# Kernel tuning notes

Measured on AMD Instinct MI355X. Metric: run time of the kernel, lower is better.

Reference implementation:

```python
import jax, jax.numpy as jnp
import numpy as np

B, C, H, W = 4, 256, 64, 64
PD = 32  # projection_dim = in_channels // projection_ratio


def setup_inputs() -> dict:
    key = jax.random.key(0)
    ks = jax.random.split(key, 7)
    x = jax.random.normal(ks[0], (B, C, H, W), dtype=jnp.float32)
    Wq = jax.random.normal(ks[1], (PD, C), dtype=jnp.float32) * (1.0 / np.sqrt(C))
    bq = jax.random.normal(ks[2], (PD,), dtype=jnp.float32) * 0.01
    Wk = jax.random.normal(ks[3], (PD, C), dtype=jnp.float32) * (1.0 / np.sqrt(C))
    bk = jax.random.normal(ks[4], (PD,), dtype=jnp.float32) * 0.01
    Wv = jax.random.normal(ks[5], (C, C), dtype=jnp.float32) * (1.0 / np.sqrt(C))
    bv = jax.random.normal(ks[6], (C,), dtype=jnp.float32) * 0.01
    gamma = jnp.float32(1.0)
    return {"x": x, "Wq": Wq, "bq": bq, "Wk": Wk, "bk": bk, "Wv": Wv, "bv": bv, "gamma": gamma}


def reference(x, Wq, bq, Wk, bk, Wv, bv, gamma):
    b, c, h, w = x.shape
    xf = x.reshape(b, c, h * w)                      # [B, C, N]
    q = jnp.einsum('dc,bcn->bnd', Wq, xf) + bq       # [B, N, PD]
    k = jnp.einsum('dc,bcn->bdn', Wk, xf) + bk[:, None]   # [B, PD, N]
    v = jnp.einsum('ec,bcn->ben', Wv, xf) + bv[:, None]   # [B, C, N]
    scores = jnp.einsum('bnd,bdm->bnm', q, k)        # [B, N, N] (no scaling, per original)
    attn = jax.nn.softmax(scores, axis=-1)           # softmax over keys
    out = jnp.einsum('bcn,bmn->bcm', v, attn)        # v @ attn^T -> [B, C, N]
    out = out.reshape(b, c, h, w)
    return gamma * out + x
```

## Files before the change

### kernel.cpp

```cpp
#include <hip/hip_runtime.h>
#include <stdint.h>

typedef _Float16 half_t;
typedef __attribute__((ext_vector_type(8))) _Float16 f16x8;
typedef __attribute__((ext_vector_type(4))) _Float16 f16x4;
typedef __attribute__((ext_vector_type(2))) __fp16 fp16x2;
typedef __attribute__((ext_vector_type(4))) float f32x4;
typedef __attribute__((ext_vector_type(16))) float f32x16;
typedef __attribute__((ext_vector_type(4))) uint32_t u32x4;
typedef __attribute__((ext_vector_type(2))) int i32x2;

#define DEVI __device__ __forceinline__

static constexpr int Bn = 4, Cc = 256, Nn = 4096, PD = 32;
static constexpr float L2E = 1.44269504089f;

__device__ half_t g_Q[(size_t)Bn * Nn * PD];
__device__ half_t g_K[(size_t)Bn * Nn * PD];
__device__ half_t g_V[(size_t)Bn * Cc * Nn];

DEVI f16x8 cvt8(float4 a, float4 b) {
    f16x8 r;
    r[0] = (_Float16)a.x; r[1] = (_Float16)a.y; r[2] = (_Float16)a.z; r[3] = (_Float16)a.w;
    r[4] = (_Float16)b.x; r[5] = (_Float16)b.y; r[6] = (_Float16)b.z; r[7] = (_Float16)b.w;
    return r;
}

DEVI uint32_t pkrtz(float a, float b) {
    fp16x2 h = __builtin_amdgcn_cvt_pkrtz(a, b);
    return __builtin_bit_cast(uint32_t, h);
}

DEVI float asf(int u) { return __builtin_bit_cast(float, u); }
DEVI int   asi(float f) { return __builtin_bit_cast(int, f); }

DEVI i32x2 pl32swap(int a, int b) {
    return __builtin_amdgcn_permlane32_swap(a, b, false, false);
}

DEVI void gll16(const void* g, void* l) {
    auto gp = (const __attribute__((address_space(1))) uint32_t*)(uintptr_t)g;
    auto lp = (__attribute__((address_space(3))) uint32_t*)(uintptr_t)l;
    __builtin_amdgcn_global_load_lds(gp, lp, 16, 0, 0);
}

__global__ __launch_bounds__(256, 1) void proj_kernel(
    const float* __restrict__ x,
    const float* __restrict__ Wq, const float* __restrict__ bq,
    const float* __restrict__ Wk, const float* __restrict__ bk,
    const float* __restrict__ Wv, const float* __restrict__ bv)
{
    __shared__ __align__(16) half_t xt[64 * 40];

    const int b    = blockIdx.x >> 6;
    const int n0   = (blockIdx.x & 63) * 64;
    const int t    = threadIdx.x;
    const int w    = t >> 6;
    const int lane = t & 63;
    const int l15  = lane & 15, g = lane >> 4;

    f32x4 qk_acc[4] = {};
    f32x4 v_acc[4][4] = {};

    const float* wrow_qk = (w < 2) ? (Wq + (size_t)(16 * w + l15) * Cc)
                                   : (Wk + (size_t)(16 * (w - 2) + l15) * Cc);

    for (int cs = 0; cs < 8; ++cs) {
        const int c0 = cs * 32;
        {
            const int nl = t & 63;
            const int cg = t >> 6;
            const float* xp = x + ((size_t)(b * Cc + c0 + cg * 8)) * Nn + n0 + nl;
            float f[8];
#pragma unroll
            for (int q = 0; q < 8; ++q) f[q] = xp[(size_t)q * Nn];
            f16x4 h0, h1;
#pragma unroll
            for (int q = 0; q < 4; ++q) { h0[q] = (_Float16)f[q]; h1[q] = (_Float16)f[q + 4]; }
            *(f16x4*)&xt[nl * 40 + cg * 8]     = h0;
            *(f16x4*)&xt[nl * 40 + cg * 8 + 4] = h1;
        }
        __syncthreads();

        f16x8 xf[4];
#pragma unroll
        for (int nf = 0; nf < 4; ++nf)
            xf[nf] = *(const f16x8*)&xt[(nf * 16 + l15) * 40 + g * 8];

        {
            const float* wp = wrow_qk + c0 + g * 8;
            const f16x8 af = cvt8(*(const float4*)wp, *(const float4*)(wp + 4));
#pragma unroll
            for (int nt = 0; nt < 4; ++nt)
                qk_acc[nt] = __builtin_amdgcn_mfma_f32_16x16x32_f16(af, xf[nt], qk_acc[nt], 0, 0, 0);
        }
#pragma unroll
        for (int et = 0; et < 4; ++et) {
            const int e = (w * 4 + et) * 16 + l15;
            const float* wp = Wv + (size_t)e * Cc + c0 + g * 8;
            const f16x8 wf = cvt8(*(const float4*)wp, *(const float4*)(wp + 4));
#pragma unroll
            for (int nf = 0; nf < 4; ++nf)
                v_acc[et][nf] = __builtin_amdgcn_mfma_f32_16x16x32_f16(xf[nf], wf, v_acc[et][nf], 0, 0, 0);
        }
        __syncthreads();
    }

    {
        const float* bias = (w < 2) ? bq : bk;
        const int dbase = 16 * (w & 1) + 4 * g;
        float bb[4];
#pragma unroll
        for (int r = 0; r < 4; ++r) bb[r] = bias[dbase + r];
        half_t* dst = (w < 2) ? g_Q : g_K;
#pragma unroll
        for (int nt = 0; nt < 4; ++nt) {
            const int n = n0 + nt * 16 + l15;
            f16x4 h;
#pragma unroll
            for (int r = 0; r < 4; ++r) h[r] = (_Float16)(qk_acc[nt][r] + bb[r]);
            *(f16x4*)&dst[((size_t)b * Nn + n) * PD + dbase] = h;
        }
    }
#pragma unroll
    for (int et = 0; et < 4; ++et) {
        const int e = (w * 4 + et) * 16 + l15;
        const float bve = bv[e];
#pragma unroll
        for (int nf = 0; nf < 4; ++nf) {
            const int n = n0 + nf * 16 + 4 * g;
            f16x4 h;
#pragma unroll
            for (int r = 0; r < 4; ++r) h[r] = (_Float16)(v_acc[et][nf][r] + bve);
            *(f16x4*)&g_V[((size_t)b * Cc + e) * Nn + n] = h;
        }
    }
}

__global__ __launch_bounds__(512, 2) void attn_kernel(
    const float* __restrict__ x, const float* __restrict__ gamma_p, float* __restrict__ out)
{
    __shared__ __align__(16) half_t V_lds[2][256 * 128];
    __shared__ float mx[2][4][32];
    __shared__ float lx[2][4][32];

    const int blk = blockIdx.x;
    const int grp = blk & 7;
    const int b   = grp >> 1;
    const int mt  = ((blk >> 3) << 1) | (grp & 1);

    const int t    = threadIdx.x;
    const int w    = t >> 6;
    const int lane = t & 63;
    const int l31  = lane & 31;
    const int hi   = lane >> 5;
    const int kk   = w & 3;
    const int mh   = w >> 2;
    const int mrow0 = mt * 64 + mh * 32;

    const half_t* Kb  = g_K + (size_t)b * Nn * PD;
    const half_t* Vbg = g_V + (size_t)b * Cc * Nn;

    const half_t* qp = g_Q + ((size_t)b * Nn + mrow0 + l31) * PD + hi * 8;
    const f16x8 q0 = *(const f16x8*)qp;
    const f16x8 q1 = *(const f16x8*)(qp + 16);

    const int vr = w * 4 + (lane >> 4);
    const half_t* vb = Vbg + (size_t)vr * Nn + (((lane & 15) ^ (vr & 7)) * 8);

    const int e7   = l31 & 7;
    const int off0 = (((kk * 4) + hi) ^ e7) * 8;
    const int off1 = (((kk * 4) + 2 + hi) ^ e7) * 8;

    f32x16 acc[8] = {};
    float run_m = -1e30f, run_l = 0.f;
    const f32x16 zero16 = {};

    f32x16 s;
    f16x8 kq0, kq1;

    {
        const half_t* kp0 = Kb + (size_t)(kk * 32 + l31) * PD + hi * 8;
        const f16x8 ka = *(const f16x8*)kp0;
        const f16x8 kb = *(const f16x8*)(kp0 + 16);
        s = __builtin_amdgcn_mfma_f32_32x32x16_f16(ka, q0, zero16, 0, 0, 0);
        s = __builtin_amdgcn_mfma_f32_32x32x16_f16(kb, q1, s, 0, 0, 0);
    }
#pragma unroll
    for (int rr = 0; rr < 8; ++rr)
        gll16(vb + (size_t)rr * 32 * Nn, &V_lds[0][rr * 4096 + w * 512]);
    __builtin_amdgcn_sched_barrier(0);
    const half_t* kp = Kb + (size_t)(128 + kk * 32 + l31) * PD + hi * 8;
    kq0 = *(const f16x8*)kp;
    kq1 = *(const f16x8*)(kp + 16);
    __builtin_amdgcn_sched_barrier(0);

    constexpr int NT = Nn / 128;
    for (int i = 0; i < NT; ++i) {
        const int buf = i & 1;
        const bool more = (i + 1 < NT);

        asm volatile("s_waitcnt vmcnt(2)" ::: "memory");
        __builtin_amdgcn_s_barrier();
        __builtin_amdgcn_sched_barrier(0);

        float tm = s[0];
#pragma unroll
        for (int r = 1; r < 16; ++r) tm = fmaxf(tm, s[r]);
        {
            const i32x2 rr = pl32swap(asi(tm), asi(tm));
            tm = fmaxf(asf(rr[0]), asf(rr[1]));
        }
        float alpha = 1.f;
        if (__any(tm > run_m + 8.f)) {
            const float nm = fmaxf(run_m, tm);
            alpha = __builtin_amdgcn_exp2f((run_m - nm) * L2E);
            run_m = nm;
            float a16[16];
#pragma unroll
            for (int r = 0; r < 16; ++r)
                a16[r] = __shfl(alpha, (r & 3) + 8 * (r >> 2) + 4 * hi);
#pragma unroll
            for (int et = 0; et < 8; ++et)
#pragma unroll
                for (int r = 0; r < 16; ++r) acc[et][r] *= a16[r];
        }

        const float nms = run_m * L2E;
        float p[16];
#pragma unroll
        for (int r = 0; r < 16; ++r)
            p[r] = __builtin_amdgcn_exp2f(s[r] * L2E - nms);
        float rs = (((p[0] + p[1]) + (p[2] + p[3])) + ((p[4] + p[5]) + (p[6] + p[7])))
                 + (((p[8] + p[9]) + (p[10] + p[11])) + ((p[12] + p[13]) + (p[14] + p[15])));
        {
            const i32x2 rr = pl32swap(asi(rs), asi(rs));
            rs = asf(rr[0]) + asf(rr[1]);
        }
        run_l = run_l * alpha + rs;

        f16x8 pa0, pa1;
        {
            const i32x2 r0 = pl32swap((int)pkrtz(p[0], p[1]), (int)pkrtz(p[4], p[5]));
            const i32x2 r1 = pl32swap((int)pkrtz(p[2], p[3]), (int)pkrtz(p[6], p[7]));
            u32x4 d0 = {(uint32_t)r0[0], (uint32_t)r1[0], (uint32_t)r0[1], (uint32_t)r1[1]};
            pa0 = __builtin_bit_cast(f16x8, d0);
            const i32x2 r2 = pl32swap((int)pkrtz(p[8], p[9]),   (int)pkrtz(p[12], p[13]));
            const i32x2 r3 = pl32swap((int)pkrtz(p[10], p[11]), (int)pkrtz(p[14], p[15]));
            u32x4 d1 = {(uint32_t)r2[0], (uint32_t)r3[0], (uint32_t)r2[1], (uint32_t)r3[1]};
            pa1 = __builtin_bit_cast(f16x8, d1);
        }

        if (more) {
#pragma unroll
            for (int rr = 0; rr < 8; ++rr)
                gll16(vb + 128 + (size_t)rr * 32 * Nn, &V_lds[buf ^ 1][rr * 4096 + w * 512]);
            vb += 128;
        }
        __builtin_amdgcn_sched_barrier(0);

        __builtin_amdgcn_s_setprio(1);
#pragma unroll
        for (int et = 0; et < 8; ++et) {
            const int rowb = (et * 32 + l31) * 128;
            const f16x8 vf0 = *(const f16x8*)&V_lds[buf][rowb + off0];
            const f16x8 vf1 = *(const f16x8*)&V_lds[buf][rowb + off1];
            acc[et] = __builtin_amdgcn_mfma_f32_32x32x16_f16(pa0, vf0, acc[et], 0, 0, 0);
            acc[et] = __builtin_amdgcn_mfma_f32_32x32x16_f16(pa1, vf1, acc[et], 0, 0, 0);
        }
        __builtin_amdgcn_s_setprio(0);

        if (more) {
            s = __builtin_amdgcn_mfma_f32_32x32x16_f16(kq0, q0, zero16, 0, 0, 0);
            s = __builtin_amdgcn_mfma_f32_32x32x16_f16(kq1, q1, s, 0, 0, 0);
            kp += 128 * PD;
            if (i + 2 >= NT) kp = Kb + (size_t)(kk * 32 + l31) * PD + hi * 8;
            kq0 = *(const f16x8*)kp;
            kq1 = *(const f16x8*)(kp + 16);
            __builtin_amdgcn_sched_barrier(0);
        }
    }

    if (lane < 32) { mx[mh][kk][l31] = run_m; lx[mh][kk][l31] = run_l; }
    __syncthreads();

    float sc16[16], li16[16];
    {
        const float m0 = mx[mh][0][l31], m1 = mx[mh][1][l31];
        const float m2 = mx[mh][2][l31], m3 = mx[mh][3][l31];
        const float M  = fmaxf(fmaxf(m0, m1), fmaxf(m2, m3));
        const float L  = lx[mh][0][l31] * __builtin_amdgcn_exp2f((m0 - M) * L2E)
                       + lx[mh][1][l31] * __builtin_amdgcn_exp2f((m1 - M) * L2E)
                       + lx[mh][2][l31] * __builtin_amdgcn_exp2f((m2 - M) * L2E)
                       + lx[mh][3][l31] * __builtin_amdgcn_exp2f((m3 - M) * L2E);
        const float ssf = __builtin_amdgcn_exp2f((run_m - M) * L2E);
        const float inv = 1.0f / L;
#pragma unroll
        for (int r = 0; r < 16; ++r) {
            const int src = (r & 3) + 8 * (r >> 2) + 4 * hi;
            sc16[r] = __shfl(ssf, src);
            li16[r] = __shfl(inv, src);
        }
    }
    __syncthreads();

    const float gm = gamma_p[0];
    float4* mrg = (float4*)&V_lds[0][0];
#pragma unroll
    for (int h = 0; h < 2; ++h) {
#pragma unroll
        for (int j = 0; j < 4; ++j) {
            const int et = h * 4 + j;
#pragma unroll
            for (int q = 0; q < 4; ++q) {
                float4 v;
                v.x = acc[et][4 * q + 0] * sc16[4 * q + 0];
                v.y = acc[et][4 * q + 1] * sc16[4 * q + 1];
                v.z = acc[et][4 * q + 2] * sc16[4 * q + 2];
                v.w = acc[et][4 * q + 3] * sc16[4 * q + 3];
                mrg[((w * 4 + j) * 4 + q) * 64 + lane] = v;
            }
        }
        __syncthreads();
        {
            const int et = h * 4 + kk;
            const int e  = et * 32 + l31;
#pragma unroll
            for (int q = 0; q < 4; ++q) {
                float4 s0 = mrg[(((mh * 4 + 0) * 4 + kk) * 4 + q) * 64 + lane];
                float4 s1 = mrg[(((mh * 4 + 1) * 4 + kk) * 4 + q) * 64 + lane];
                float4 s2 = mrg[(((mh * 4 + 2) * 4 + kk) * 4 + q) * 64 + lane];
                float4 s3 = mrg[(((mh * 4 + 3) * 4 + kk) * 4 + q) * 64 + lane];
                const size_t idx = ((size_t)b * Cc + e) * Nn + mrow0 + 8 * q + 4 * hi;
                const float4 xin = *(const float4*)&x[idx];
                float4 o;
                o.x = gm * (s0.x + s1.x + s2.x + s3.x) * li16[4 * q + 0] + xin.x;
                o.y = gm * (s0.y + s1.y + s2.y + s3.y) * li16[4 * q + 1] + xin.y;
                o.z = gm * (s0.z + s1.z + s2.z + s3.z) * li16[4 * q + 2] + xin.z;
                o.w = gm * (s0.w + s1.w + s2.w + s3.w) * li16[4 * q + 3] + xin.w;
                *(float4*)&out[idx] = o;
            }
        }
        __syncthreads();
    }
}

extern "C" void kernel_launch(void* const* d_in, const int* in_sizes, int n_in,
                              void* d_out, int out_size, void* d_ws, size_t ws_size,
                              hipStream_t stream) {
    (void)in_sizes; (void)n_in; (void)out_size; (void)d_ws; (void)ws_size;
    const float* x  = (const float*)d_in[0];
    const float* Wq = (const float*)d_in[1];
    const float* bq = (const float*)d_in[2];
    const float* Wk = (const float*)d_in[3];
    const float* bk = (const float*)d_in[4];
    const float* Wv = (const float*)d_in[5];
    const float* bv = (const float*)d_in[6];
    const float* gm = (const float*)d_in[7];
    float* out = (float*)d_out;

    proj_kernel<<<256, 256, 0, stream>>>(x, Wq, bq, Wk, bk, Wv, bv);
    attn_kernel<<<256, 512, 0, stream>>>(x, gm, out);
}
```

Baseline: 81.34 us.

## Software-pipeline softmax of next tile between halves of PV MFMAs

Restructures the flash-attention main loop so the QK scores and softmax/pack for tile i+1 are computed while the PV MFMAs for tile i run. The softmax is split into the middle of the PV MFMA sequence to interleave VALU exp work with matrix ops. The accumulator rescale is deferred to the start of the next iteration, and the final tile is peeled out of the loop. This raises register pressure, since the next P fragments and scores stay live alongside the accumulators.

```diff
diff --git a/kernel.cpp b/kernel.cpp
--- a/kernel.cpp
+++ b/kernel.cpp
@@ -176,15 +176,62 @@
     float run_m = -1e30f, run_l = 0.f;
     const f32x16 zero16 = {};
 
-    f32x16 s;
+    f16x8 pa0, pa1;
     f16x8 kq0, kq1;
+    float alpha = 1.f;
+    bool  needscale = false;
+
+    auto softmax_pack = [&](const f32x16& sn, f16x8& o0, f16x8& o1) {
+        float m01 = fmaxf(sn[0], sn[1]),   m23 = fmaxf(sn[2], sn[3]);
+        float m45 = fmaxf(sn[4], sn[5]),   m67 = fmaxf(sn[6], sn[7]);
+        float m89 = fmaxf(sn[8], sn[9]),   mab = fmaxf(sn[10], sn[11]);
+        float mcd = fmaxf(sn[12], sn[13]), mef = fmaxf(sn[14], sn[15]);
+        float tm = fmaxf(fmaxf(fmaxf(m01, m23), fmaxf(m45, m67)),
+                         fmaxf(fmaxf(m89, mab), fmaxf(mcd, mef)));
+        {
+            const i32x2 rr = pl32swap(asi(tm), asi(tm));
+            tm = fmaxf(asf(rr[0]), asf(rr[1]));
+        }
+        needscale = __any(tm > run_m + 8.f);
+        if (needscale) {
+            const float nm = fmaxf(run_m, tm);
+            alpha = __builtin_amdgcn_exp2f((run_m - nm) * L2E);
+            run_m = nm;
+        } else {
+            alpha = 1.f;
+        }
+        const float nms = run_m * L2E;
+        float p[16];
+#pragma unroll
+        for (int r = 0; r < 16; ++r)
+            p[r] = __builtin_amdgcn_exp2f(sn[r] * L2E - nms);
+        float rs = (((p[0] + p[1]) + (p[2] + p[3])) + ((p[4] + p[5]) + (p[6] + p[7])))
+                 + (((p[8] + p[9]) + (p[10] + p[11])) + ((p[12] + p[13]) + (p[14] + p[15])));
+        {
+            const i32x2 rr = pl32swap(asi(rs), asi(rs));
+            rs = asf(rr[0]) + asf(rr[1]);
+        }
+        run_l = run_l * alpha + rs;
+        {
+            const i32x2 r0 = pl32swap((int)pkrtz(p[0], p[1]), (int)pkrtz(p[4], p[5]));
+            const i32x2 r1 = pl32swap((int)pkrtz(p[2], p[3]), (int)pkrtz(p[6], p[7]));
+            u32x4 d0 = {(uint32_t)r0[0], (uint32_t)r1[0], (uint32_t)r0[1], (uint32_t)r1[1]};
+            o0 = __builtin_bit_cast(f16x8, d0);
+            const i32x2 r2 = pl32swap((int)pkrtz(p[8], p[9]),   (int)pkrtz(p[12], p[13]));
+            const i32x2 r3 = pl32swap((int)pkrtz(p[10], p[11]), (int)pkrtz(p[14], p[15]));
+            u32x4 d1 = {(uint32_t)r2[0], (uint32_t)r3[0], (uint32_t)r2[1], (uint32_t)r3[1]};
+            o1 = __builtin_bit_cast(f16x8, d1);
+        }
+    };
 
     {
         const half_t* kp0 = Kb + (size_t)(kk * 32 + l31) * PD + hi * 8;
         const f16x8 ka = *(const f16x8*)kp0;
         const f16x8 kb = *(const f16x8*)(kp0 + 16);
-        s = __builtin_amdgcn_mfma_f32_32x32x16_f16(ka, q0, zero16, 0, 0, 0);
-        s = __builtin_amdgcn_mfma_f32_32x32x16_f16(kb, q1, s, 0, 0, 0);
+        f32x16 s0 = __builtin_amdgcn_mfma_f32_32x32x16_f16(ka, q0, zero16, 0, 0, 0);
+        s0 = __builtin_amdgcn_mfma_f32_32x32x16_f16(kb, q1, s0, 0, 0, 0);
+        softmax_pack(s0, pa0, pa1);
+        needscale = false;
     }
 #pragma unroll
     for (int rr = 0; rr < 8; ++rr)
@@ -196,69 +243,78 @@
     __builtin_amdgcn_sched_barrier(0);
 
     constexpr int NT = Nn / 128;
-    for (int i = 0; i < NT; ++i) {
+    for (int i = 0; i < NT - 1; ++i) {
         const int buf = i & 1;
-        const bool more = (i + 1 < NT);
 
         asm volatile("s_waitcnt vmcnt(2)" ::: "memory");
         __builtin_amdgcn_s_barrier();
         __builtin_amdgcn_sched_barrier(0);
 
-        float tm = s[0];
-#pragma unroll
-        for (int r = 1; r < 16; ++r) tm = fmaxf(tm, s[r]);
-        {
-            const i32x2 rr = pl32swap(asi(tm), asi(tm));
-            tm = fmaxf(asf(rr[0]), asf(rr[1]));
-        }
-        float alpha = 1.f;
-        if (__any(tm > run_m + 8.f)) {
-            const float nm = fmaxf(run_m, tm);
-            alpha = __builtin_amdgcn_exp2f((run_m - nm) * L2E);
-            run_m = nm;
-            float a16[16];
-#pragma unroll
-            for (int r = 0; r < 16; ++r)
-                a16[r] = __shfl(alpha, (r & 3) + 8 * (r >> 2) + 4 * hi);
-#pragma unroll
-            for (int et = 0; et < 8; ++et)
-#pragma unroll
-                for (int r = 0; r < 16; ++r) acc[et][r] *= a16[r];
-        }
-
-        const float nms = run_m * L2E;
-        float p[16];
-#pragma unroll
-        for (int r = 0; r < 16; ++r)
-            p[r] = __builtin_amdgcn_exp2f(s[r] * L2E - nms);
-        float rs = (((p[0] + p[1]) + (p[2] + p[3])) + ((p[4] + p[5]) + (p[6] + p[7])))
-                 + (((p[8] + p[9]) + (p[10] + p[11])) + ((p[12] + p[13]) + (p[14] + p[15])));
-        {
-            const i32x2 rr = pl32swap(asi(rs), asi(rs));
-            rs = asf(rr[0]) + asf(rr[1]);
-        }
-        run_l = run_l * alpha + rs;
-
-        f16x8 pa0, pa1;
-        {
-            const i32x2 r0 = pl32swap((int)pkrtz(p[0], p[1]), (int)pkrtz(p[4], p[5]));
-            const i32x2 r1 = pl32swap((int)pkrtz(p[2], p[3]), (int)pkrtz(p[6], p[7]));
-            u32x4 d0 = {(uint32_t)r0[0], (uint32_t)r1[0], (uint32_t)r0[1], (uint32_t)r1[1]};
-            pa0 = __builtin_bit_cast(f16x8, d0);
-            const i32x2 r2 = pl32swap((int)pkrtz(p[8], p[9]),   (int)pkrtz(p[12], p[13]));
-            const i32x2 r3 = pl32swap((int)pkrtz(p[10], p[11]), (int)pkrtz(p[14], p[15]));
-            u32x4 d1 = {(uint32_t)r2[0], (uint32_t)r3[0], (uint32_t)r2[1], (uint32_t)r3[1]};
-            pa1 = __builtin_bit_cast(f16x8, d1);
-        }
-
-        if (more) {
-#pragma unroll
-            for (int rr = 0; rr < 8; ++rr)
-                gll16(vb + 128 + (size_t)rr * 32 * Nn, &V_lds[buf ^ 1][rr * 4096 + w * 512]);
-            vb += 128;
-        }
+        if (needscale) {
+#pragma unroll
+            for (int r = 0; r < 16; ++r) {
+                const float ar = __shfl(alpha, (r & 3) + 8 * (r >> 2) + 4 * hi);
+#pragma unroll
+                for (int et = 0; et < 8; ++et) acc[et][r] *= ar;
+            }
+        }
+
+        f32x16 sn = __builtin_amdgcn_mfma_f32_32x32x16_f16(kq0, q0, zero16, 0, 0, 0);
+        sn = __builtin_amdgcn_mfma_f32_32x32x16_f16(kq1, q1, sn, 0, 0, 0);
+
+#pragma unroll
+        for (int rr = 0; rr < 8; ++rr)
+            gll16(vb + 128 + (size_t)rr * 32 * Nn, &V_lds[buf ^ 1][rr * 4096 + w * 512]);
+        vb += 128;
+
+        __builtin_amdgcn_s_setprio(1);
+#pragma unroll
+        for (int et = 0; et < 4; ++et) {
+            const int rowb = (et * 32 + l31) * 128;
+            const f16x8 vf0 = *(const f16x8*)&V_lds[buf][rowb + off0];
+            const f16x8 vf1 = *(const f16x8*)&V_lds[buf][rowb + off1];
+            acc[et] = __builtin_amdgcn_mfma_f32_32x32x16_f16(pa0, vf0, acc[et], 0, 0, 0);
+            acc[et] = __builtin_amdgcn_mfma_f32_32x32x16_f16(pa1, vf1, acc[et], 0, 0, 0);
+        }
+        __builtin_amdgcn_s_setprio(0);
+
+        f16x8 pn0, pn1;
+        softmax_pack(sn, pn0, pn1);
+
+        __builtin_amdgcn_s_setprio(1);
+#pragma unroll
+        for (int et = 4; et < 8; ++et) {
+            const int rowb = (et * 32 + l31) * 128;
+            const f16x8 vf0 = *(const f16x8*)&V_lds[buf][rowb + off0];
+            const f16x8 vf1 = *(const f16x8*)&V_lds[buf][rowb + off1];
+            acc[et] = __builtin_amdgcn_mfma_f32_32x32x16_f16(pa0, vf0, acc[et], 0, 0, 0);
+            acc[et] = __builtin_amdgcn_mfma_f32_32x32x16_f16(pa1, vf1, acc[et], 0, 0, 0);
+        }
+        __builtin_amdgcn_s_setprio(0);
+
+        pa0 = pn0;
+        pa1 = pn1;
+
+        kp += 128 * PD;
+        if (i + 2 >= NT) kp = Kb + (size_t)(kk * 32 + l31) * PD + hi * 8;
+        kq0 = *(const f16x8*)kp;
+        kq1 = *(const f16x8*)(kp + 16);
         __builtin_amdgcn_sched_barrier(0);
-
+    }
+
+    {
+        const int buf = (NT - 1) & 1;
+        asm volatile("s_waitcnt vmcnt(2)" ::: "memory");
+        __builtin_amdgcn_s_barrier();
+        __builtin_amdgcn_sched_barrier(0);
+        if (needscale) {
+#pragma unroll
+            for (int r = 0; r < 16; ++r) {
+                const float ar = __shfl(alpha, (r & 3) + 8 * (r >> 2) + 4 * hi);
+#pragma unroll
+                for (int et = 0; et < 8; ++et) acc[et][r] *= ar;
+            }
+        }
         __builtin_amdgcn_s_setprio(1);
 #pragma unroll
         for (int et = 0; et < 8; ++et) {
@@ -269,16 +325,6 @@
             acc[et] = __builtin_amdgcn_mfma_f32_32x32x16_f16(pa1, vf1, acc[et], 0, 0, 0);
         }
         __builtin_amdgcn_s_setprio(0);
-
-        if (more) {
-            s = __builtin_amdgcn_mfma_f32_32x32x16_f16(kq0, q0, zero16, 0, 0, 0);
-            s = __builtin_amdgcn_mfma_f32_32x32x16_f16(kq1, q1, s, 0, 0, 0);
-            kp += 128 * PD;
-            if (i + 2 >= NT) kp = Kb + (size_t)(kk * 32 + l31) * PD + hi * 8;
-            kq0 = *(const f16x8*)kp;
-            kq1 = *(const f16x8*)(kp + 16);
-            __builtin_amdgcn_sched_barrier(0);
-        }
     }
 
     if (lane < 32) { mx[mh][kk][l31] = run_m; lx[mh][kk][l31] = run_l; }
```

Measured after the change: 91.26 us. +12.2%, slower.

## Shrink attention blocks to 32 query rows, single-buffer V, fold log2e into Q

Applied to the files above, without the earlier changes.

The attention kernel now runs 512 blocks of 4 waves, each covering 32 query rows instead of 64. The V tile in LDS drops from double to single buffering, with an extra barrier before the next tile is fetched. The projection kernel pre-multiplies Q by log2(e), so the softmax exp2 no longer needs a per-element multiply, and the rescale threshold is adjusted to match. This trades twice the K/V traffic per query and less load/compute overlap for smaller blocks, less LDS per block and possibly higher occupancy.

```diff
diff --git a/kernel.cpp b/kernel.cpp
--- a/kernel.cpp
+++ b/kernel.cpp
@@ -14,6 +14,7 @@
 
 static constexpr int Bn = 4, Cc = 256, Nn = 4096, PD = 32;
 static constexpr float L2E = 1.44269504089f;
+static constexpr float THR = 11.5416f;
 
 __device__ half_t g_Q[(size_t)Bn * Nn * PD];
 __device__ half_t g_K[(size_t)Bn * Nn * PD];
@@ -108,6 +109,7 @@
 
     {
         const float* bias = (w < 2) ? bq : bk;
+        const float scl   = (w < 2) ? L2E : 1.f;
         const int dbase = 16 * (w & 1) + 4 * g;
         float bb[4];
 #pragma unroll
@@ -118,7 +120,7 @@
             const int n = n0 + nt * 16 + l15;
             f16x4 h;
 #pragma unroll
-            for (int r = 0; r < 4; ++r) h[r] = (_Float16)(qk_acc[nt][r] + bb[r]);
+            for (int r = 0; r < 4; ++r) h[r] = (_Float16)((qk_acc[nt][r] + bb[r]) * scl);
             *(f16x4*)&dst[((size_t)b * Nn + n) * PD + dbase] = h;
         }
     }
@@ -137,12 +139,12 @@
     }
 }
 
-__global__ __launch_bounds__(512, 2) void attn_kernel(
+__global__ __launch_bounds__(256, 2) void attn_kernel(
     const float* __restrict__ x, const float* __restrict__ gamma_p, float* __restrict__ out)
 {
-    __shared__ __align__(16) half_t V_lds[2][256 * 128];
-    __shared__ float mx[2][4][32];
-    __shared__ float lx[2][4][32];
+    __shared__ __align__(16) half_t V_lds[256 * 128];
+    __shared__ float mx[4][32];
+    __shared__ float lx[4][32];
 
     const int blk = blockIdx.x;
     const int grp = blk & 7;
@@ -154,9 +156,8 @@
     const int lane = t & 63;
     const int l31  = lane & 31;
     const int hi   = lane >> 5;
-    const int kk   = w & 3;
-    const int mh   = w >> 2;
-    const int mrow0 = mt * 64 + mh * 32;
+    const int kk   = w;
+    const int mrow0 = mt * 32;
 
     const half_t* Kb  = g_K + (size_t)b * Nn * PD;
     const half_t* Vbg = g_V + (size_t)b * Cc * Nn;
@@ -187,8 +188,8 @@
         s = __builtin_amdgcn_mfma_f32_32x32x16_f16(kb, q1, s, 0, 0, 0);
     }
 #pragma unroll
-    for (int rr = 0; rr < 8; ++rr)
-        gll16(vb + (size_t)rr * 32 * Nn, &V_lds[0][rr * 4096 + w * 512]);
+    for (int rr = 0; rr < 16; ++rr)
+        gll16(vb + (size_t)rr * 16 * Nn, &V_lds[rr * 2048 + w * 512]);
     __builtin_amdgcn_sched_barrier(0);
     const half_t* kp = Kb + (size_t)(128 + kk * 32 + l31) * PD + hi * 8;
     kq0 = *(const f16x8*)kp;
@@ -197,7 +198,6 @@
 
     constexpr int NT = Nn / 128;
     for (int i = 0; i < NT; ++i) {
-        const int buf = i & 1;
         const bool more = (i + 1 < NT);
 
         asm volatile("s_waitcnt vmcnt(2)" ::: "memory");
@@ -212,9 +212,9 @@
             tm = fmaxf(asf(rr[0]), asf(rr[1]));
         }
         float alpha = 1.f;
-        if (__any(tm > run_m + 8.f)) {
+        if (__any(tm > run_m + THR)) {
             const float nm = fmaxf(run_m, tm);
-            alpha = __builtin_amdgcn_exp2f((run_m - nm) * L2E);
+            alpha = __builtin_amdgcn_exp2f(run_m - nm);
             run_m = nm;
             float a16[16];
 #pragma unroll
@@ -226,11 +226,10 @@
                 for (int r = 0; r < 16; ++r) acc[et][r] *= a16[r];
         }
 
-        const float nms = run_m * L2E;
         float p[16];
 #pragma unroll
         for (int r = 0; r < 16; ++r)
-            p[r] = __builtin_amdgcn_exp2f(s[r] * L2E - nms);
+            p[r] = __builtin_amdgcn_exp2f(s[r] - run_m);
         float rs = (((p[0] + p[1]) + (p[2] + p[3])) + ((p[4] + p[5]) + (p[6] + p[7])))
                  + (((p[8] + p[9]) + (p[10] + p[11])) + ((p[12] + p[13]) + (p[14] + p[15])));
         {
@@ -251,26 +250,27 @@
             pa1 = __builtin_bit_cast(f16x8, d1);
         }
 
-        if (more) {
-#pragma unroll
-            for (int rr = 0; rr < 8; ++rr)
-                gll16(vb + 128 + (size_t)rr * 32 * Nn, &V_lds[buf ^ 1][rr * 4096 + w * 512]);
-            vb += 128;
-        }
-        __builtin_amdgcn_sched_barrier(0);
-
         __builtin_amdgcn_s_setprio(1);
 #pragma unroll
         for (int et = 0; et < 8; ++et) {
             const int rowb = (et * 32 + l31) * 128;
-            const f16x8 vf0 = *(const f16x8*)&V_lds[buf][rowb + off0];
-            const f16x8 vf1 = *(const f16x8*)&V_lds[buf][rowb + off1];
+            const f16x8 vf0 = *(const f16x8*)&V_lds[rowb + off0];
+            const f16x8 vf1 = *(const f16x8*)&V_lds[rowb + off1];
             acc[et] = __builtin_amdgcn_mfma_f32_32x32x16_f16(pa0, vf0, acc[et], 0, 0, 0);
             acc[et] = __builtin_amdgcn_mfma_f32_32x32x16_f16(pa1, vf1, acc[et], 0, 0, 0);
         }
         __builtin_amdgcn_s_setprio(0);
 
+        __builtin_amdgcn_s_barrier();
+        __builtin_amdgcn_sched_barrier(0);
+
         if (more) {
+            vb += 128;
+#pragma unroll
+            for (int rr = 0; rr < 16; ++rr)
+                gll16(vb + (size_t)rr * 16 * Nn, &V_lds[rr * 2048 + w * 512]);
+            __builtin_amdgcn_sched_barrier(0);
+
             s = __builtin_amdgcn_mfma_f32_32x32x16_f16(kq0, q0, zero16, 0, 0, 0);
             s = __builtin_amdgcn_mfma_f32_32x32x16_f16(kq1, q1, s, 0, 0, 0);
             kp += 128 * PD;
@@ -281,19 +281,19 @@
         }
     }
 
-    if (lane < 32) { mx[mh][kk][l31] = run_m; lx[mh][kk][l31] = run_l; }
+    if (lane < 32) { mx[kk][l31] = run_m; lx[kk][l31] = run_l; }
     __syncthreads();
 
     float sc16[16], li16[16];
     {
-        const float m0 = mx[mh][0][l31], m1 = mx[mh][1][l31];
-        const float m2 = mx[mh][2][l31], m3 = mx[mh][3][l31];
+        const float m0 = mx[0][l31], m1 = mx[1][l31];
+        const float m2 = mx[2][l31], m3 = mx[3][l31];
         const float M  = fmaxf(fmaxf(m0, m1), fmaxf(m2, m3));
-        const float L  = lx[mh][0][l31] * __builtin_amdgcn_exp2f((m0 - M) * L2E)
-                       + lx[mh][1][l31] * __builtin_amdgcn_exp2f((m1 - M) * L2E)
-                       + lx[mh][2][l31] * __builtin_amdgcn_exp2f((m2 - M) * L2E)
-                       + lx[mh][3][l31] * __builtin_amdgcn_exp2f((m3 - M) * L2E);
-        const float ssf = __builtin_amdgcn_exp2f((run_m - M) * L2E);
+        const float L  = lx[0][l31] * __builtin_amdgcn_exp2f(m0 - M)
+                       + lx[1][l31] * __builtin_amdgcn_exp2f(m1 - M)
+                       + lx[2][l31] * __builtin_amdgcn_exp2f(m2 - M)
+                       + lx[3][l31] * __builtin_amdgcn_exp2f(m3 - M);
+        const float ssf = __builtin_amdgcn_exp2f(run_m - M);
         const float inv = 1.0f / L;
 #pragma unroll
         for (int r = 0; r < 16; ++r) {
@@ -305,7 +305,7 @@
     __syncthreads();
 
     const float gm = gamma_p[0];
-    float4* mrg = (float4*)&V_lds[0][0];
+    float4* mrg = (float4*)&V_lds[0];
 #pragma unroll
     for (int h = 0; h < 2; ++h) {
 #pragma unroll
@@ -327,10 +327,10 @@
             const int e  = et * 32 + l31;
 #pragma unroll
             for (int q = 0; q < 4; ++q) {
-                float4 s0 = mrg[(((mh * 4 + 0) * 4 + kk) * 4 + q) * 64 + lane];
-                float4 s1 = mrg[(((mh * 4 + 1) * 4 + kk) * 4 + q) * 64 + lane];
-                float4 s2 = mrg[(((mh * 4 + 2) * 4 + kk) * 4 + q) * 64 + lane];
-                float4 s3 = mrg[(((mh * 4 + 3) * 4 + kk) * 4 + q) * 64 + lane];
+                float4 s0 = mrg[(((0 * 4 + kk) * 4 + q)) * 64 + lane];
+                float4 s1 = mrg[(((1 * 4 + kk) * 4 + q)) * 64 + lane];
+                float4 s2 = mrg[(((2 * 4 + kk) * 4 + q)) * 64 + lane];
+                float4 s3 = mrg[(((3 * 4 + kk) * 4 + q)) * 64 + lane];
                 const size_t idx = ((size_t)b * Cc + e) * Nn + mrow0 + 8 * q + 4 * hi;
                 const float4 xin = *(const float4*)&x[idx];
                 float4 o;
@@ -360,5 +360,5 @@
     float* out = (float*)d_out;
 
     proj_kernel<<<256, 256, 0, stream>>>(x, Wq, bq, Wk, bk, Wv, bv);
-    attn_kernel<<<256, 512, 0, stream>>>(x, gm, out);
-}
+    attn_kernel<<<512, 256, 0, stream>>>(x, gm, out);
+}
```

Result: slower. 100.3 us (+23.3%).
